# Kernel optimization log

Hardware: AMD Instinct MI355X
Metric: run time of the kernel (lower is better)

Reference implementation:

```python
import jax, jax.numpy as jnp
import numpy as np

# ---- config (from Mamba2Config defaults) ----
D_MODEL = 1024
D_STATE = 128
D_CONV = 4
EXPAND = 2
HEADDIM = 64
D_INNER = EXPAND * D_MODEL          # 2048
NHEADS = D_INNER // HEADDIM         # 32
CONV_DIM = D_INNER + 2 * D_STATE    # 2304 (ngroups=1)
D_IN_PROJ = 2 * D_INNER + 2 * D_STATE + NHEADS  # 4384
INTER = ((int(D_MODEL * 8 / 3) + 63) // 64) * 64  # 2752
EPS = 1e-6
BATCH, SEQLEN = 2, 1024


def rmsnorm(x, w):
    return x * jax.lax.rsqrt(jnp.mean(x * x, axis=-1, keepdims=True) + EPS) * w


def setup_inputs() -> dict:
    key = jax.random.key(0)
    ks = jax.random.split(key, 16)
    s = 0.02
    return {
        "hidden_states": jax.random.normal(ks[0], (BATCH, SEQLEN, D_MODEL), jnp.float32),
        "norm_w": jnp.ones((D_MODEL,), jnp.float32),
        "in_proj_w": jax.random.normal(ks[1], (D_IN_PROJ, D_MODEL), jnp.float32) * s,
        "conv_w": jax.random.normal(ks[2], (CONV_DIM, D_CONV), jnp.float32) * 0.2,
        "conv_b": jnp.zeros((CONV_DIM,), jnp.float32),
        "dt_bias": jax.random.normal(ks[3], (NHEADS,), jnp.float32) * 0.5,
        "A_log": jnp.log(jax.random.uniform(ks[4], (NHEADS,), jnp.float32, 1.0, 16.0)),
        "D": jnp.ones((NHEADS,), jnp.float32) + jax.random.normal(ks[5], (NHEADS,), jnp.float32) * 0.05,
        "ssm_norm_w": jnp.ones((D_INNER,), jnp.float32),
        "out_proj_w": jax.random.normal(ks[6], (D_MODEL, D_INNER), jnp.float32) * s,
        "post_norm_w": jnp.ones((D_MODEL,), jnp.float32),
        "gate_w": jax.random.normal(ks[7], (INTER, D_MODEL), jnp.float32) * s,
        "up_w": jax.random.normal(ks[8], (INTER, D_MODEL), jnp.float32) * s,
        "down_w": jax.random.normal(ks[9], (D_MODEL, INTER), jnp.float32) * s,
    }


def _mixer(u, in_proj_w, conv_w, conv_b, dt_bias, A_log, D, ssm_norm_w, out_proj_w):
    b, l, _ = u.shape
    zxbcdt = u @ in_proj_w.T                              # (b,l,4384)
    z = zxbcdt[..., :D_INNER]                             # gate
    xBC = zxbcdt[..., D_INNER:D_INNER + CONV_DIM]
    dt = zxbcdt[..., -NHEADS:]

    # causal depthwise conv1d (kernel D_CONV) + SiLU
    xp = jnp.pad(xBC, ((0, 0), (D_CONV - 1, 0), (0, 0)))
    xBC = sum(xp[:, k:k + l, :] * conv_w[:, k] for k in range(D_CONV)) + conv_b
    xBC = jax.nn.silu(xBC)

    xs = xBC[..., :D_INNER].reshape(b, l, NHEADS, HEADDIM)   # (b,l,h,p)
    Bm = xBC[..., D_INNER:D_INNER + D_STATE]                  # (b,l,n)
    Cm = xBC[..., -D_STATE:]                                  # (b,l,n)

    dt = jax.nn.softplus(dt + dt_bias)                        # (b,l,h)
    A = -jnp.exp(A_log)                                       # (h,)

    def step(h, inp):
        dt_t, x_t, B_t, C_t = inp                             # (b,h),(b,h,p),(b,n),(b,n)
        dA = jnp.exp(dt_t * A)                                # (b,h)
        h = h * dA[..., None, None] + jnp.einsum('bh,bhp,bn->bhpn', dt_t, x_t, B_t)
        y_t = jnp.einsum('bhpn,bn->bhp', h, C_t)
        return h, y_t

    h0 = jnp.zeros((b, NHEADS, HEADDIM, D_STATE), u.dtype)
    xsT = (jnp.moveaxis(dt, 1, 0), jnp.moveaxis(xs, 1, 0),
           jnp.moveaxis(Bm, 1, 0), jnp.moveaxis(Cm, 1, 0))
    _, yT = jax.lax.scan(step, h0, xsT)                       # (l,b,h,p)
    y = jnp.moveaxis(yT, 0, 1) + D[None, None, :, None] * xs  # skip term
    y = y.reshape(b, l, D_INNER)

    # gated RMSNorm (norm_before_gate=False): normalize y*silu(z)
    y = rmsnorm(y * jax.nn.silu(z), ssm_norm_w)
    return y @ out_proj_w.T


def reference(hidden_states, norm_w, in_proj_w, conv_w, conv_b, dt_bias, A_log, D,
              ssm_norm_w, out_proj_w, post_norm_w, gate_w, up_w, down_w):
    res = hidden_states
    h = rmsnorm(hidden_states, norm_w)
    h = _mixer(h, in_proj_w, conv_w, conv_b, dt_bias, A_log, D, ssm_norm_w, out_proj_w)
    x = res + h
    res = x
    h = rmsnorm(x, post_norm_w)
    h = (jax.nn.silu(h @ gate_w.T) * (h @ up_w.T)) @ down_w.T  # SwiGLU MLP
    return res + h
```

## Files before the change

kernel.cpp:

```cpp
#include <hip/hip_runtime.h>
#include <hip/hip_bf16.h>

#define SEQLEN   1024
#define NTOK     2048
#define DMODEL   1024
#define DSTATE   128
#define DINNER   2048
#define NHEADS   32
#define HEADDIM  64
#define CONVDIM  2304
#define DINPROJ  4384
#define INTER    2752
#define Q        64
#define NCHUNK   16

typedef __hip_bfloat16 bf16;
typedef unsigned short ushort_t;
typedef __attribute__((ext_vector_type(8))) short bf16x8;
typedef __attribute__((ext_vector_type(4))) float f32x4;
typedef __attribute__((ext_vector_type(4))) unsigned short u16x4;

__device__ __forceinline__ float bf2f(bf16 x) { return __bfloat162float(x); }
__device__ __forceinline__ float bfu2f(ushort_t u) {
    return __uint_as_float(((unsigned)u) << 16);
}
__device__ __forceinline__ ushort_t f2bfu(float x) {
    union { bf16 h; ushort_t u; } c; c.h = __float2bfloat16(x); return c.u;
}

__device__ __forceinline__ void glds16(const void* g, void* l) {
    __builtin_amdgcn_global_load_lds(
        (const __attribute__((address_space(1))) void*)g,
        (__attribute__((address_space(3))) void*)l, 16, 0, 0);
}

__device__ inline float block_reduce_sum(float v) {
    __shared__ float red[4];
    #pragma unroll
    for (int off = 32; off >= 1; off >>= 1) v += __shfl_down(v, off);
    int lane = threadIdx.x & 63, w = threadIdx.x >> 6;
    if (lane == 0) red[w] = v;
    __syncthreads();
    return red[0] + red[1] + red[2] + red[3];
}

__global__ __launch_bounds__(256) void f2bf_kernel(
    const float* __restrict__ src, ushort_t* __restrict__ dst, int n)
{
    const int i = (blockIdx.x * 256 + threadIdx.x) * 4;
    if (i < n) {
        const f32x4 v = *(const f32x4*)(src + i);
        u16x4 o;
        #pragma unroll
        for (int k = 0; k < 4; k++) o[k] = f2bfu(v[k]);
        *(u16x4*)(dst + i) = o;
    }
}

#define NWOP (DMODEL * DINNER)
#define NWG  (INTER * DMODEL)
__global__ __launch_bounds__(256) void convert_weights_kernel(
    const float* __restrict__ wop, const float* __restrict__ wg,
    const float* __restrict__ wu, const float* __restrict__ wd,
    ushort_t* __restrict__ dWop, ushort_t* __restrict__ dWgu,
    ushort_t* __restrict__ dWdn)
{
    const int i4 = (blockIdx.x * 256 + threadIdx.x) * 4;
    const float* src;
    ushort_t* dst;
    if (i4 < NWOP) { src = wop + i4; dst = dWop + i4; }
    else if (i4 < NWOP + NWG) {
        const int e = i4 - NWOP, row = e >> 10, col = e & 1023;
        src = wg + e; dst = dWgu + ((size_t)(2 * row) << 10) + col;
    } else if (i4 < NWOP + 2 * NWG) {
        const int e = i4 - NWOP - NWG, row = e >> 10, col = e & 1023;
        src = wu + e; dst = dWgu + ((size_t)(2 * row + 1) << 10) + col;
    } else if (i4 < NWOP + 3 * NWG) {
        const int e = i4 - NWOP - 2 * NWG;
        src = wd + e; dst = dWdn + e;
    } else return;
    const f32x4 v = *(const f32x4*)src;
    u16x4 o;
    #pragma unroll
    for (int k = 0; k < 4; k++) o[k] = f2bfu(v[k]);
    *(u16x4*)dst = o;
}

__global__ __launch_bounds__(256) void rmsnorm1024_kernel(
    const float* __restrict__ x, const float* __restrict__ w, bf16* __restrict__ out)
{
    const int token = blockIdx.x, t = threadIdx.x;
    float v[4]; float ss = 0.f;
    #pragma unroll
    for (int i = 0; i < 4; i++) {
        v[i] = x[(size_t)token * DMODEL + t * 4 + i];
        ss += v[i] * v[i];
    }
    ss = block_reduce_sum(ss);
    const float scale = rsqrtf(ss * (1.0f / DMODEL) + 1e-6f);
    #pragma unroll
    for (int i = 0; i < 4; i++)
        out[(size_t)token * DMODEL + t * 4 + i] =
            __float2bfloat16(v[i] * scale * w[t * 4 + i]);
}

template <int EPI, int MT, int NT>
__global__ __launch_bounds__(256) void gemm_bf(
    const bf16* __restrict__ A, const bf16* __restrict__ W,
    float* __restrict__ Cf, const float* __restrict__ resid_f,
    bf16* __restrict__ out_bf, int M, int N, int K)
{
    __shared__ ushort_t As[MT * 64];
    __shared__ ushort_t Bs[NT * 64];
    const int tid = threadIdx.x;
    const int w = tid >> 6, lane = tid & 63;
    const int m0 = blockIdx.y * MT, n0 = blockIdx.x * NT;

    const int srow = tid >> 3;
    const int scol = (((tid & 7) ^ (srow & 7)) * 8);
    const bf16* Agp[MT / 32];
    const bf16* Wgp[NT / 32];
    #pragma unroll
    for (int i = 0; i < MT / 32; i++)
        Agp[i] = A + (size_t)(m0 + i * 32 + srow) * K + scol;
    #pragma unroll
    for (int i = 0; i < NT / 32; i++) {
        const int nr = n0 + i * 32 + srow;
        Wgp[i] = W + (size_t)(nr < N ? nr : 0) * K + scol;
    }
    ushort_t* lA = &As[w * 512];
    ushort_t* lB = &Bs[w * 512];

    const int wy = w >> 1, wx = w & 1;
    const int fr = lane & 15;
    const int fq = lane >> 4;
    constexpr int MI = MT / 32;
    constexpr int NJ = NT / 32;
    f32x4 acc[MI][NJ];
    #pragma unroll
    for (int i = 0; i < MI; i++)
        #pragma unroll
        for (int j = 0; j < NJ; j++)
            acc[i][j] = (f32x4){0.f, 0.f, 0.f, 0.f};

    for (int k0 = 0; k0 < K; k0 += 64) {
        __syncthreads();
        #pragma unroll
        for (int i = 0; i < MT / 32; i++)
            glds16(Agp[i] + k0, lA + i * 2048);
        #pragma unroll
        for (int i = 0; i < NT / 32; i++)
            glds16(Wgp[i] + k0, lB + i * 2048);
        __syncthreads();
        #pragma unroll
        for (int ks = 0; ks < 2; ks++) {
            bf16x8 af[MI], bfv[NJ];
            #pragma unroll
            for (int i = 0; i < MI; i++) {
                const int r = wy * (MT / 2) + i * 16 + fr;
                const int g = ks * 4 + fq;
                af[i] = *(const bf16x8*)&As[r * 64 + ((g ^ (r & 7)) * 8)];
            }
            #pragma unroll
            for (int j = 0; j < NJ; j++) {
                const int r = wx * (NT / 2) + j * 16 + fr;
                const int g = ks * 4 + fq;
                bfv[j] = *(const bf16x8*)&Bs[r * 64 + ((g ^ (r & 7)) * 8)];
            }
            #pragma unroll
            for (int i = 0; i < MI; i++)
                #pragma unroll
                for (int j = 0; j < NJ; j++)
                    acc[i][j] = __builtin_amdgcn_mfma_f32_16x16x32_bf16(
                        af[i], bfv[j], acc[i][j], 0, 0, 0);
        }
    }

    #pragma unroll
    for (int i = 0; i < MI; i++) {
        #pragma unroll
        for (int j = 0; j < NJ; j++) {
            const int mb = m0 + wy * (MT / 2) + i * 16 + (lane >> 4) * 4;
            const int nn = n0 + wx * (NT / 2) + j * 16 + (lane & 15);
            if (nn < N) {
                #pragma unroll
                for (int r = 0; r < 4; r++) {
                    if (EPI == 2) {
                        const float g = acc[i][j][r];
                        const float u = __shfl_xor(g, 1);
                        if (!(lane & 1)) {
                            const float a = (g / (1.f + expf(-g))) * u;
                            out_bf[(size_t)(mb + r) * (N / 2) + (nn >> 1)] =
                                __float2bfloat16(a);
                        }
                    } else {
                        const size_t idx = (size_t)(mb + r) * N + nn;
                        float v = acc[i][j][r];
                        if (EPI == 1) v += resid_f[idx];
                        Cf[idx] = v;
                    }
                }
            }
        }
    }
}

__global__ __launch_bounds__(256) void conv_silu_kernel(
    const float* __restrict__ zx, const float* __restrict__ cw,
    const float* __restrict__ cb, ushort_t* __restrict__ out)
{
    const int idx = blockIdx.x * 256 + threadIdx.x;
    if (idx >= NTOK * CONVDIM) return;
    const int c = idx % CONVDIM;
    const int token = idx / CONVDIM;
    const int l = token & (SEQLEN - 1);
    float acc = cb[c];
    #pragma unroll
    for (int k = 0; k < 4; k++) {
        const int ls = l - 3 + k;
        if (ls >= 0)
            acc += zx[(size_t)(token - 3 + k) * DINPROJ + DINNER + c] * cw[c * 4 + k];
    }
    out[(size_t)token * CONVDIM + c] = f2bfu(acc / (1.f + expf(-acc)));
}

__global__ __launch_bounds__(256) void dt_softplus_kernel(
    const float* __restrict__ zx, const float* __restrict__ dtb,
    float* __restrict__ out)
{
    const int idx = blockIdx.x * 256 + threadIdx.x;
    const int h = idx & (NHEADS - 1);
    const int token = idx >> 5;
    float v = zx[(size_t)token * DINPROJ + (DINNER + CONVDIM) + h] + dtb[h];
    out[idx] = (v > 20.f) ? v : log1pf(expf(v));
}

__global__ __launch_bounds__(256) void chunk_state_kernel(
    const ushort_t* __restrict__ cvb, const float* __restrict__ dtb,
    const float* __restrict__ A_log, float* __restrict__ ccum,
    ushort_t* __restrict__ Sbuf)
{
    const int bx = blockIdx.x;
    const int bh = bx >> 4, c = bx & 15;
    const int b = bh >> 5, h = bh & 31;
    const int t = threadIdx.x;
    const int w = t >> 6, lane = t & 63;
    const int wy = w >> 1, wx = w & 1;
    const int fr = lane & 15, fk = (lane >> 4) * 8, cr = (lane >> 4) * 4;
    const int tok0 = b * SEQLEN + c * Q;
    const float A = -expf(A_log[h]);

    __shared__ ushort_t sXT[64 * 88];
    __shared__ ushort_t sBT[128 * 88];
    __shared__ float sW[64];

    if (t < 64) {
        const float d = dtb[(size_t)(tok0 + t) * NHEADS + h];
        float s = d;
        #pragma unroll
        for (int off = 1; off < 64; off <<= 1) {
            const float up = __shfl_up(s, off);
            if (t >= off) s += up;
        }
        const float total = __shfl(s, 63);
        sW[t] = expf(A * (total - s)) * d;
        if (t == 63) ccum[bh * NCHUNK + c] = A * total;
    }
    __syncthreads();

    for (int i = t; i < 64 * 64; i += 256) {
        const int l = i >> 6, p = i & 63;
        const float v = bfu2f(cvb[(size_t)(tok0 + l) * CONVDIM + h * HEADDIM + p]);
        sXT[p * 88 + l] = f2bfu(sW[l] * v);
    }
    for (int i = t; i < 128 * 64; i += 256) {
        const int l = i >> 7, n = i & 127;
        sBT[n * 88 + l] = cvb[(size_t)(tok0 + l) * CONVDIM + DINNER + n];
    }
    __syncthreads();

    f32x4 acc[2][4];
    #pragma unroll
    for (int i = 0; i < 2; i++)
        #pragma unroll
        for (int j = 0; j < 4; j++)
            acc[i][j] = (f32x4){0.f, 0.f, 0.f, 0.f};
    #pragma unroll
    for (int k0 = 0; k0 < 64; k0 += 32) {
        bf16x8 af[2], bfv[4];
        #pragma unroll
        for (int i = 0; i < 2; i++)
            af[i] = *(const bf16x8*)&sXT[(wy * 32 + i * 16 + fr) * 88 + fk + k0];
        #pragma unroll
        for (int j = 0; j < 4; j++)
            bfv[j] = *(const bf16x8*)&sBT[(wx * 64 + j * 16 + fr) * 88 + fk + k0];
        #pragma unroll
        for (int i = 0; i < 2; i++)
            #pragma unroll
            for (int j = 0; j < 4; j++)
                acc[i][j] = __builtin_amdgcn_mfma_f32_16x16x32_bf16(
                    af[i], bfv[j], acc[i][j], 0, 0, 0);
    }
    const size_t slot = (size_t)(bh * NCHUNK + c) * 64 * 128;
    #pragma unroll
    for (int i = 0; i < 2; i++) {
        #pragma unroll
        for (int j = 0; j < 4; j++) {
            #pragma unroll
            for (int r = 0; r < 4; r++) {
                const int pr = wy * 32 + i * 16 + cr + r;
                const int nn = wx * 64 + j * 16 + fr;
                Sbuf[slot + pr * 128 + nn] = f2bfu(acc[i][j][r]);
            }
        }
    }
}

__global__ __launch_bounds__(256) void stitch_kernel(
    const float* __restrict__ ccum, ushort_t* __restrict__ Sbuf)
{
    const int bh = blockIdx.x;
    const int t = threadIdx.x, p = t >> 2, q = t & 3;
    float H[32];
    #pragma unroll
    for (int j = 0; j < 32; j++) H[j] = 0.f;
    for (int c = 0; c < NCHUNK; c++) {
        const float P = expf(ccum[bh * NCHUNK + c]);
        const size_t slot = ((size_t)(bh * NCHUNK + c) * 64 + p) * 128;
        #pragma unroll
        for (int jj = 0; jj < 8; jj++) {
            const u16x4 sv4 = *(const u16x4*)&Sbuf[slot + q * 4 + 16 * jj];
            u16x4 hv4;
            #pragma unroll
            for (int k = 0; k < 4; k++) hv4[k] = f2bfu(H[jj * 4 + k]);
            *(u16x4*)&Sbuf[slot + q * 4 + 16 * jj] = hv4;
            #pragma unroll
            for (int k = 0; k < 4; k++)
                H[jj * 4 + k] = P * H[jj * 4 + k] + bfu2f(sv4[k]);
        }
    }
}

__global__ __launch_bounds__(256) void chunk_scan_mfma_kernel(
    const ushort_t* __restrict__ cvb, const float* __restrict__ dtb,
    const float* __restrict__ A_log, const float* __restrict__ Dh,
    const ushort_t* __restrict__ Sbuf, bf16* __restrict__ ybuf)
{
    const int bx = blockIdx.x;
    const int bh = bx >> 4, c = bx & 15;
    const int b = bh >> 5, h = bh & 31;
    const int t = threadIdx.x;
    const int w = t >> 6, lane = t & 63;
    const int wy = w >> 1, wx = w & 1;
    const int fr = lane & 15;
    const int fk = (lane >> 4) * 8;
    const int cr = (lane >> 4) * 4;
    const int tok0 = b * SEQLEN + c * Q;
    const float A = -expf(A_log[h]);
    const float Dv = Dh[h];

    __shared__ ushort_t sB[64 * 136];
    __shared__ ushort_t sC[64 * 136];
    __shared__ ushort_t sH[64 * 136];
    __shared__ ushort_t sXT[64 * 72];
    __shared__ ushort_t sM[64 * 72];
    __shared__ float    sCum[64];
    __shared__ float    sDtv[64];

    for (int i = t; i < 64 * 32; i += 256) {
        const int row = i >> 5, col = (i & 31) * 4;
        const size_t base = (size_t)(tok0 + row) * CONVDIM;
        *(u16x4*)&sB[row * 136 + col] = *(const u16x4*)&cvb[base + DINNER + col];
        *(u16x4*)&sC[row * 136 + col] = *(const u16x4*)&cvb[base + DINNER + DSTATE + col];
    }
    for (int i = t; i < 64 * 32; i += 256) {
        const int p = i >> 5, l0 = (i & 31) * 2;
        const ushort_t x0 = cvb[(size_t)(tok0 + l0)     * CONVDIM + h * HEADDIM + p];
        const ushort_t x1 = cvb[(size_t)(tok0 + l0 + 1) * CONVDIM + h * HEADDIM + p];
        *(unsigned*)&sXT[p * 72 + l0] = ((unsigned)x1 << 16) | x0;
    }
    {
        const size_t slot = (size_t)(bh * NCHUNK + c) * 64 * 128;
        for (int i = t * 4; i < 64 * 128; i += 1024) {
            const int row = i >> 7, col = i & 127;
            *(u16x4*)&sH[row * 136 + col] = *(const u16x4*)&Sbuf[slot + row * 128 + col];
        }
    }
    if (t < 64) {
        const float d = dtb[(size_t)(tok0 + t) * NHEADS + h];
        float s = d;
        #pragma unroll
        for (int off = 1; off < 64; off <<= 1) {
            const float up = __shfl_up(s, off);
            if (t >= off) s += up;
        }
        sCum[t] = A * s;
        sDtv[t] = d;
    }
    __syncthreads();

    f32x4 accg[2][2];
    #pragma unroll
    for (int i = 0; i < 2; i++)
        #pragma unroll
        for (int j = 0; j < 2; j++)
            accg[i][j] = (f32x4){0.f, 0.f, 0.f, 0.f};
    #pragma unroll
    for (int k0 = 0; k0 < 128; k0 += 32) {
        bf16x8 af[2], bfv[2];
        #pragma unroll
        for (int i = 0; i < 2; i++)
            af[i] = *(const bf16x8*)&sC[(wy * 32 + i * 16 + fr) * 136 + fk + k0];
        #pragma unroll
        for (int j = 0; j < 2; j++)
            bfv[j] = *(const bf16x8*)&sB[(wx * 32 + j * 16 + fr) * 136 + fk + k0];
        #pragma unroll
        for (int i = 0; i < 2; i++)
            #pragma unroll
            for (int j = 0; j < 2; j++)
                accg[i][j] = __builtin_amdgcn_mfma_f32_16x16x32_bf16(
                    af[i], bfv[j], accg[i][j], 0, 0, 0);
    }
    __syncthreads();

    #pragma unroll
    for (int i = 0; i < 2; i++) {
        #pragma unroll
        for (int j = 0; j < 2; j++) {
            #pragma unroll
            for (int r = 0; r < 4; r++) {
                const int l  = wy * 32 + i * 16 + cr + r;
                const int jc = wx * 32 + j * 16 + fr;
                const float v = (jc <= l)
                    ? accg[i][j][r] * expf(sCum[l] - sCum[jc]) * sDtv[jc] : 0.f;
                sM[l * 72 + jc] = f2bfu(v);
            }
        }
    }
    for (int i = t; i < 64 * 32; i += 256) {
        const int row = i >> 5, col = (i & 31) * 4;
        const float sc = expf(sCum[row]);
        u16x4 v = *(const u16x4*)&sC[row * 136 + col];
        #pragma unroll
        for (int k = 0; k < 4; k++) v[k] = f2bfu(bfu2f(v[k]) * sc);
        *(u16x4*)&sC[row * 136 + col] = v;
    }
    __syncthreads();

    f32x4 accy[2][2];
    #pragma unroll
    for (int i = 0; i < 2; i++)
        #pragma unroll
        for (int j = 0; j < 2; j++)
            accy[i][j] = (f32x4){0.f, 0.f, 0.f, 0.f};
    #pragma unroll
    for (int k0 = 0; k0 < 64; k0 += 32) {
        bf16x8 af[2], bfv[2];
        #pragma unroll
        for (int i = 0; i < 2; i++)
            af[i] = *(const bf16x8*)&sM[(wy * 32 + i * 16 + fr) * 72 + fk + k0];
        #pragma unroll
        for (int j = 0; j < 2; j++)
            bfv[j] = *(const bf16x8*)&sXT[(wx * 32 + j * 16 + fr) * 72 + fk + k0];
        #pragma unroll
        for (int i = 0; i < 2; i++)
            #pragma unroll
            for (int j = 0; j < 2; j++)
                accy[i][j] = __builtin_amdgcn_mfma_f32_16x16x32_bf16(
                    af[i], bfv[j], accy[i][j], 0, 0, 0);
    }
    #pragma unroll
    for (int k0 = 0; k0 < 128; k0 += 32) {
        bf16x8 af[2], bfv[2];
        #pragma unroll
        for (int i = 0; i < 2; i++)
            af[i] = *(const bf16x8*)&sC[(wy * 32 + i * 16 + fr) * 136 + fk + k0];
        #pragma unroll
        for (int j = 0; j < 2; j++)
            bfv[j] = *(const bf16x8*)&sH[(wx * 32 + j * 16 + fr) * 136 + fk + k0];
        #pragma unroll
        for (int i = 0; i < 2; i++)
            #pragma unroll
            for (int j = 0; j < 2; j++)
                accy[i][j] = __builtin_amdgcn_mfma_f32_16x16x32_bf16(
                    af[i], bfv[j], accy[i][j], 0, 0, 0);
    }

    #pragma unroll
    for (int i = 0; i < 2; i++) {
        #pragma unroll
        for (int j = 0; j < 2; j++) {
            #pragma unroll
            for (int r = 0; r < 4; r++) {
                const int l = wy * 32 + i * 16 + cr + r;
                const int p = wx * 32 + j * 16 + fr;
                const float x = bfu2f(sXT[p * 72 + l]);
                ybuf[(size_t)(tok0 + l) * DINNER + h * HEADDIM + p] =
                    __float2bfloat16(accy[i][j][r] + Dv * x);
            }
        }
    }
}

__global__ __launch_bounds__(256) void gated_rmsnorm_kernel(
    const bf16* __restrict__ y, const float* __restrict__ zx,
    const float* __restrict__ w, bf16* __restrict__ out)
{
    const int token = blockIdx.x, t = threadIdx.x;
    const bf16* yr = y + (size_t)token * DINNER;
    const float* zr = zx + (size_t)token * DINPROJ;
    float v[8]; float ss = 0.f;
    #pragma unroll
    for (int i = 0; i < 8; i++) {
        const int idx = t * 8 + i;
        const float zz = zr[idx];
        const float val = bf2f(yr[idx]) * (zz / (1.f + expf(-zz)));
        v[i] = val; ss += val * val;
    }
    ss = block_reduce_sum(ss);
    const float scale = rsqrtf(ss * (1.0f / DINNER) + 1e-6f);
    #pragma unroll
    for (int i = 0; i < 8; i++) {
        const int idx = t * 8 + i;
        out[(size_t)token * DINNER + idx] =
            __float2bfloat16(v[i] * scale * w[idx]);
    }
}

extern "C" void kernel_launch(void* const* d_in, const int* in_sizes, int n_in,
                              void* d_out, int out_size, void* d_ws, size_t ws_size,
                              hipStream_t stream) {
    const float* hidden     = (const float*)d_in[0];
    const float* norm_w     = (const float*)d_in[1];
    const float* in_proj_w  = (const float*)d_in[2];
    const float* conv_w     = (const float*)d_in[3];
    const float* conv_b     = (const float*)d_in[4];
    const float* dt_bias    = (const float*)d_in[5];
    const float* A_log      = (const float*)d_in[6];
    const float* Dh         = (const float*)d_in[7];
    const float* ssm_norm_w = (const float*)d_in[8];
    const float* out_proj_w = (const float*)d_in[9];
    const float* post_norm_w= (const float*)d_in[10];
    const float* gate_w     = (const float*)d_in[11];
    const float* up_w       = (const float*)d_in[12];
    const float* down_w     = (const float*)d_in[13];
    float* out = (float*)d_out;

    float* ws = (float*)d_ws;
    bf16*  h_norm = (bf16*)(ws);
    float* zx     = ws + 1048576;
    ushort_t* cvb = (ushort_t*)(ws + 10027008);
    float* dtb    = ws + 14745600;
    float* ccum   = ws + 14811136;
    ushort_t* Sbuf= (ushort_t*)(ws + 14812160);
    float* xbuf   = ws + 19006464;
    bf16*  ybuf   = (bf16*)(ws + 21103616);
    bf16*  ynorm  = (bf16*)(ws + 22152192);
    ushort_t* Wip = (ushort_t*)(ws + 10027008);
    ushort_t* Wop = (ushort_t*)(ws + 1048576);
    ushort_t* Wgu = (ushort_t*)(ws + 2097152);
    ushort_t* Wdn = (ushort_t*)(ws + 4915200);
    bf16*  act    = (bf16*)(ws + 6324224);
    bf16*  h2     = h_norm;

    f2bf_kernel<<<4384, 256, 0, stream>>>(in_proj_w, Wip, DINPROJ * DMODEL);
    rmsnorm1024_kernel<<<NTOK, 256, 0, stream>>>(hidden, norm_w, h_norm);
    gemm_bf<0, 128, 128><<<dim3(35, 16), 256, 0, stream>>>(h_norm, (const bf16*)Wip, zx,
        nullptr, nullptr, NTOK, DINPROJ, DMODEL);
    conv_silu_kernel<<<(NTOK * CONVDIM) / 256, 256, 0, stream>>>(zx, conv_w, conv_b, cvb);
    dt_softplus_kernel<<<(NTOK * NHEADS) / 256, 256, 0, stream>>>(zx, dt_bias, dtb);
    chunk_state_kernel<<<1024, 256, 0, stream>>>(cvb, dtb, A_log, ccum, Sbuf);
    stitch_kernel<<<64, 256, 0, stream>>>(ccum, Sbuf);
    chunk_scan_mfma_kernel<<<1024, 256, 0, stream>>>(cvb, dtb, A_log, Dh, Sbuf, ybuf);
    gated_rmsnorm_kernel<<<NTOK, 256, 0, stream>>>(ybuf, zx, ssm_norm_w, ynorm);
    convert_weights_kernel<<<(NWOP + 3 * NWG) / 1024, 256, 0, stream>>>(
        out_proj_w, gate_w, up_w, down_w, Wop, Wgu, Wdn);
    gemm_bf<1, 64, 64><<<dim3(16, 32), 256, 0, stream>>>(ynorm, (const bf16*)Wop, xbuf,
        hidden, nullptr, NTOK, DMODEL, DINNER);
    rmsnorm1024_kernel<<<NTOK, 256, 0, stream>>>(xbuf, post_norm_w, h2);
    gemm_bf<2, 128, 128><<<dim3(43, 16), 256, 0, stream>>>(h2, (const bf16*)Wgu,
        nullptr, nullptr, act, NTOK, 2 * INTER, DMODEL);
    gemm_bf<1, 64, 64><<<dim3(16, 32), 256, 0, stream>>>(act, (const bf16*)Wdn, out,
        xbuf, nullptr, NTOK, DMODEL, INTER);
}
```

Before: 372.9 us.

## Double-buffer GEMM LDS tiles and remap workgroups across XCDs

Each GEMM now keeps two LDS buffers and issues the global-to-LDS loads for the next K tile before computing the current one, with one barrier per iteration instead of two. This is meant to overlap memory latency with MFMA work. Workgroup IDs are also remapped so that consecutive tiles land on the same XCD, which should improve L2 reuse of shared A/W rows. The cost is twice the LDS per block, which may lower occupancy.

```diff
diff --git a/kernel.cpp b/kernel.cpp
--- a/kernel.cpp
+++ b/kernel.cpp
@@ -110,11 +110,19 @@
     float* __restrict__ Cf, const float* __restrict__ resid_f,
     bf16* __restrict__ out_bf, int M, int N, int K)
 {
-    __shared__ ushort_t As[MT * 64];
-    __shared__ ushort_t Bs[NT * 64];
+    __shared__ ushort_t As[2][MT * 64];
+    __shared__ ushort_t Bs[2][NT * 64];
     const int tid = threadIdx.x;
     const int w = tid >> 6, lane = tid & 63;
-    const int m0 = blockIdx.y * MT, n0 = blockIdx.x * NT;
+
+    const int gdx = gridDim.x, gdy = gridDim.y;
+    const int nwg = gdx * gdy;
+    const int orig = blockIdx.x + gdx * blockIdx.y;
+    const int q8 = nwg >> 3, r8 = nwg & 7;
+    const int xcd = orig & 7, lin = orig >> 3;
+    const int wg = (xcd < r8 ? xcd * (q8 + 1) : r8 * (q8 + 1) + (xcd - r8) * q8) + lin;
+    const int m0 = (wg % gdy) * MT;
+    const int n0 = (wg / gdy) * NT;
 
     const int srow = tid >> 3;
     const int scol = (((tid & 7) ^ (srow & 7)) * 8);
@@ -128,8 +136,6 @@
         const int nr = n0 + i * 32 + srow;
         Wgp[i] = W + (size_t)(nr < N ? nr : 0) * K + scol;
     }
-    ushort_t* lA = &As[w * 512];
-    ushort_t* lB = &Bs[w * 512];
 
     const int wy = w >> 1, wx = w & 1;
     const int fr = lane & 15;
@@ -143,15 +149,31 @@
         for (int j = 0; j < NJ; j++)
             acc[i][j] = (f32x4){0.f, 0.f, 0.f, 0.f};
 
-    for (int k0 = 0; k0 < K; k0 += 64) {
-        __syncthreads();
-        #pragma unroll
-        for (int i = 0; i < MT / 32; i++)
-            glds16(Agp[i] + k0, lA + i * 2048);
-        #pragma unroll
-        for (int i = 0; i < NT / 32; i++)
-            glds16(Wgp[i] + k0, lB + i * 2048);
-        __syncthreads();
+    const int nk = K >> 6;
+
+    {
+        ushort_t* sa = &As[0][w * 512];
+        ushort_t* sb = &Bs[0][w * 512];
+        #pragma unroll
+        for (int i = 0; i < MT / 32; i++) glds16(Agp[i], sa + i * 2048);
+        #pragma unroll
+        for (int i = 0; i < NT / 32; i++) glds16(Wgp[i], sb + i * 2048);
+    }
+    __syncthreads();
+
+    for (int kt = 0; kt < nk; ++kt) {
+        const int cur = kt & 1;
+        if (kt + 1 < nk) {
+            const int koff = (kt + 1) << 6;
+            ushort_t* sa = &As[cur ^ 1][w * 512];
+            ushort_t* sb = &Bs[cur ^ 1][w * 512];
+            #pragma unroll
+            for (int i = 0; i < MT / 32; i++) glds16(Agp[i] + koff, sa + i * 2048);
+            #pragma unroll
+            for (int i = 0; i < NT / 32; i++) glds16(Wgp[i] + koff, sb + i * 2048);
+        }
+        const ushort_t* ca = As[cur];
+        const ushort_t* cb = Bs[cur];
         #pragma unroll
         for (int ks = 0; ks < 2; ks++) {
             bf16x8 af[MI], bfv[NJ];
@@ -159,13 +181,13 @@
             for (int i = 0; i < MI; i++) {
                 const int r = wy * (MT / 2) + i * 16 + fr;
                 const int g = ks * 4 + fq;
-                af[i] = *(const bf16x8*)&As[r * 64 + ((g ^ (r & 7)) * 8)];
+                af[i] = *(const bf16x8*)&ca[r * 64 + ((g ^ (r & 7)) * 8)];
             }
             #pragma unroll
             for (int j = 0; j < NJ; j++) {
                 const int r = wx * (NT / 2) + j * 16 + fr;
                 const int g = ks * 4 + fq;
-                bfv[j] = *(const bf16x8*)&Bs[r * 64 + ((g ^ (r & 7)) * 8)];
+                bfv[j] = *(const bf16x8*)&cb[r * 64 + ((g ^ (r & 7)) * 8)];
             }
             #pragma unroll
             for (int i = 0; i < MI; i++)
@@ -174,6 +196,7 @@
                     acc[i][j] = __builtin_amdgcn_mfma_f32_16x16x32_bf16(
                         af[i], bfv[j], acc[i][j], 0, 0, 0);
         }
+        __syncthreads();
     }
 
     #pragma unroll
```

Result: no change. 374.9 us (+0.5%).
